# Kernel tuning notes

Hardware: AMD Instinct MI355X
Metric: run time of the kernel (lower is better)

The kernel has to match this reference:

```python
import jax, jax.numpy as jnp
import numpy as np

NJ, NS = 30000, 12000            # num job / skill nodes
E_JS, E_SJ, E_SS = 300000, 300000, 150000
SBERT, HID, OUT = 384, 128, 128
H = 2                             # GAT heads (concat=True)
NEG_SLOPE = 0.2


def setup_inputs() -> dict:
    key = jax.random.key(0)
    ks = iter(jax.random.split(key, 64))
    nrm = lambda shape, s=1.0: jax.random.normal(next(ks), shape, jnp.float32) * s
    ridx = lambda n, hi: jax.random.randint(next(ks), (n,), 0, hi, jnp.int32)
    W = 0.05  # weight scale to keep activations sane across layers
    return dict(
        x_job=nrm((NJ, SBERT)), x_skill=nrm((NS, SBERT)),
        ei_js_src=ridx(E_JS, NJ), ei_js_dst=ridx(E_JS, NS),
        ei_sj_src=ridx(E_SJ, NS), ei_sj_dst=ridx(E_SJ, NJ),
        ei_ss_src=ridx(E_SS, NS), ei_ss_dst=ridx(E_SS, NS),
        query=nrm((SBERT,)),
        W0_job=nrm((SBERT, HID), W), b0_job=jnp.zeros((HID,), jnp.float32),
        g0_job=jnp.ones((HID,), jnp.float32), be0_job=jnp.zeros((HID,), jnp.float32),
        W0_skill=nrm((SBERT, HID), W), b0_skill=jnp.zeros((HID,), jnp.float32),
        g0_skill=jnp.ones((HID,), jnp.float32), be0_skill=jnp.zeros((HID,), jnp.float32),
        gat_Ws=nrm((2, 3, HID, H * HID), W), gat_Wd=nrm((2, 3, HID, H * HID), W),
        gat_as=nrm((2, 3, H, HID), W), gat_ad=nrm((2, 3, H, HID), W),
        gat_b=jnp.zeros((2, 3, H * HID), jnp.float32),
        inter_W=nrm((2, 2, H * HID, HID), W), inter_b=jnp.zeros((2, 2, HID), jnp.float32),
        Wjf=nrm((HID, OUT), W), bjf=jnp.zeros((OUT,), jnp.float32),
        Wq=nrm((SBERT, OUT), W), bq=jnp.zeros((OUT,), jnp.float32),
    )


def _layer_norm(x, g, b):
    mu = x.mean(-1, keepdims=True)
    var = ((x - mu) ** 2).mean(-1, keepdims=True)
    return (x - mu) * jax.lax.rsqrt(var + 1e-5) * g + b


def _gat(x_src, x_dst, src, dst, Ws, Wd, a_s, a_d, bias, num_dst):
    # PyG GATConv: lin_src/lin_dst (no bias), additive attention, scatter-softmax over dst.
    hs = (x_src @ Ws).reshape(-1, H, HID)            # [Ns,H,C]
    hd = (x_dst @ Wd).reshape(-1, H, HID)            # [Nd,H,C]
    e = jax.nn.leaky_relu((hs * a_s).sum(-1)[src] + (hd * a_d).sum(-1)[dst], NEG_SLOPE)  # [E,H]
    m = jax.ops.segment_max(e, dst, num_segments=num_dst)
    p = jnp.exp(e - m[dst])
    den = jax.ops.segment_sum(p, dst, num_segments=num_dst)
    w = p / (den[dst] + 1e-16)                       # [E,H]
    out = jax.ops.segment_sum(hs[src] * w[:, :, None], dst, num_segments=num_dst)
    return out.reshape(num_dst, H * HID) + bias


def _forward(x_job, x_skill, query,
             W0_job, b0_job, g0_job, be0_job, W0_skill, b0_skill, g0_skill, be0_skill,
             gat_Ws, gat_Wd, gat_as, gat_ad, gat_b, inter_W, inter_b, Wjf, bjf, Wq, bq,
             ei_js_src, ei_js_dst, ei_sj_src, ei_sj_dst, ei_ss_src, ei_ss_dst):
    # initial per-type lin + LN + relu (dropout = identity in eval)
    xj = jax.nn.relu(_layer_norm(x_job @ W0_job + b0_job, g0_job, be0_job))
    xs = jax.nn.relu(_layer_norm(x_skill @ W0_skill + b0_skill, g0_skill, be0_skill))
    # skill->skill relation adds self loops (src == dst node type)
    loops = jnp.arange(NS, dtype=jnp.int32)
    ss_src = jnp.concatenate([ei_ss_src, loops])
    ss_dst = jnp.concatenate([ei_ss_dst, loops])
    for i in range(2):  # num_layers
        o_s = (_gat(xj, xs, ei_js_src, ei_js_dst, gat_Ws[i, 0], gat_Wd[i, 0],
                    gat_as[i, 0], gat_ad[i, 0], gat_b[i, 0], NS)
               + _gat(xs, xs, ss_src, ss_dst, gat_Ws[i, 2], gat_Wd[i, 2],
                      gat_as[i, 2], gat_ad[i, 2], gat_b[i, 2], NS))  # HeteroConv aggr='sum'
        o_j = _gat(xs, xj, ei_sj_src, ei_sj_dst, gat_Ws[i, 1], gat_Wd[i, 1],
                   gat_as[i, 1], gat_ad[i, 1], gat_b[i, 1], NJ)
        xj = jax.nn.relu(o_j @ inter_W[i, 0] + inter_b[i, 0])
        xs = jax.nn.relu(o_s @ inter_W[i, 1] + inter_b[i, 1])
    job_emb = xj @ Wjf + bjf                          # [NJ,OUT]
    q = query @ Wq + bq                               # [OUT]
    scores = job_emb @ q                              # [NJ]
    return scores, job_emb, q


def reference(x_job, x_skill, ei_js_src, ei_js_dst, ei_sj_src, ei_sj_dst,
              ei_ss_src, ei_ss_dst, query,
              W0_job, b0_job, g0_job, be0_job, W0_skill, b0_skill, g0_skill, be0_skill,
              gat_Ws, gat_Wd, gat_as, gat_ad, gat_b, inter_W, inter_b,
              Wjf, bjf, Wq, bq):
    return _forward(x_job, x_skill, query,
                    W0_job, b0_job, g0_job, be0_job, W0_skill, b0_skill, g0_skill, be0_skill,
                    gat_Ws, gat_Wd, gat_as, gat_ad, gat_b, inter_W, inter_b, Wjf, bjf, Wq, bq,
                    ei_js_src, ei_js_dst, ei_sj_src, ei_sj_dst, ei_ss_src, ei_ss_dst)
```

## Files before the change

kernel.cpp:

```cpp
#include <hip/hip_runtime.h>
#include <hip/hip_bf16.h>
#include <math.h>

#define NJ 30000
#define NS 12000
#define E_JS 300000
#define E_SJ 300000
#define E_SS 150000
#define ETOT (E_JS + E_SJ + E_SS + NS)
#define NBINS (NS + NJ + NS)
#define NBUK ((NBINS + 63) / 64)
#define SBERT 384
#define HIST_NB 512
#define SCAT_NB 120
#define CAST_MATS 10
#define CAST_BPM 48
#define PREP_CAST (CAST_MATS * CAST_BPM)
#define PREP_WA   (PREP_CAST + 12)
#define PREP_QV   PREP_WA
#define PREP_HIST (PREP_QV + 1)

static inline int cdiv(int a, int b) { return (a + b - 1) / b; }

typedef __attribute__((ext_vector_type(8))) short bf8_t;
typedef __attribute__((ext_vector_type(4))) float f4_t;
typedef unsigned short u16;

__device__ inline float bf2f(unsigned short u) {
    union { unsigned int i; float f; } z; z.i = ((unsigned int)u) << 16; return z.f;
}
__device__ inline unsigned short f2bf(float f) {
    unsigned int x = __float_as_uint(f);
    unsigned int r = (x + 0x7fffu + ((x >> 16) & 1u)) >> 16;
    return (unsigned short)r;
}

__device__ inline void edge_decode(int e, const int* js_src, const int* js_dst,
                                   const int* sj_src, const int* sj_dst,
                                   const int* ss_src, const int* ss_dst,
                                   int& src, int& bin) {
    if (e < E_JS) { src = js_src[e]; bin = js_dst[e]; }
    else if (e < E_JS + E_SJ) { int i = e - E_JS; src = sj_src[i]; bin = NS + sj_dst[i]; }
    else if (e < E_JS + E_SJ + E_SS) { int i = e - E_JS - E_SJ; src = ss_src[i]; bin = NS + NJ + ss_dst[i]; }
    else { int i = e - E_JS - E_SJ - E_SS; src = i; bin = NS + NJ + i; }
}

struct CastT { const float* src; unsigned short* dst; int K; int N; };
struct PrepArgs {
    CastT m[CAST_MATS];
    const float* Ws; const float* as_; const float* Wd; const float* ad_;
    float* wsa; float* wda; int* bcnt;
    const float* query; const float* Wq; const float* bq; float* qv;
    const int* js_src; const int* js_dst;
    const int* sj_src; const int* sj_dst;
    const int* ss_src; const int* ss_dst;
};

__global__ __launch_bounds__(256) void k_prep(PrepArgs A) {
    __shared__ float ldt[32][33];
    __shared__ int lh[NBUK];
    int b = blockIdx.x;
    if (b < PREP_CAST) {
        int mi = b / CAST_BPM, bx = b % CAST_BPM;
        CastT cm = A.m[mi];
        int tilesN = cm.N >> 5;
        int total = (cm.K >> 5) * tilesN;
        if (bx >= total) return;
        int tk = bx / tilesN, tn = bx % tilesN;
        int k0 = tk * 32, n0 = tn * 32;
        int col = threadIdx.x & 31;
        int row0 = threadIdx.x >> 5;
#pragma unroll
        for (int r = 0; r < 4; ++r) {
            int kk = row0 + r * 8;
            ldt[kk][col] = cm.src[(size_t)(k0 + kk) * cm.N + n0 + col];
        }
        __syncthreads();
#pragma unroll
        for (int r = 0; r < 4; ++r) {
            int nn = row0 + r * 8;
            cm.dst[(size_t)(n0 + nn) * cm.K + k0 + col] = f2bf(ldt[col][nn]);
        }
    } else if (b < PREP_WA) {
        int id = (b - PREP_CAST) * 256 + threadIdx.x;
        if (id >= 2 * 1536) return;
        int which = id / 1536;
        int r = id % 1536;
        int lr = r / 256;
        int kh = r % 256;
        int k = kh / 2, h = kh % 2;
        const float* W = which ? A.Wd : A.Ws;
        const float* a = which ? A.ad_ : A.as_;
        const float* wrow = W + ((size_t)(lr * 128 + k)) * 256 + h * 128;
        const float* arow = a + (size_t)(lr * 2 + h) * 128;
        float acc = 0.f;
        for (int c2 = 0; c2 < 128; ++c2) acc += wrow[c2] * arow[c2];
        (which ? A.wda : A.wsa)[lr * 256 + k * 2 + h] = acc;
    } else if (b == PREP_QV) {
        int c = threadIdx.x;
        if (c < 128) {
            float acc = A.bq[c];
            for (int k = 0; k < SBERT; ++k) acc += A.query[k] * A.Wq[(size_t)k * 128 + c];
            A.qv[c] = acc;
        }
    } else {
        int t = threadIdx.x;
        for (int i = t; i < NBUK; i += 256) lh[i] = 0;
        __syncthreads();
        int hb = b - PREP_HIST;
        for (int e = hb * 256 + t; e < ETOT; e += HIST_NB * 256) {
            int src, bin;
            edge_decode(e, A.js_src, A.js_dst, A.sj_src, A.sj_dst, A.ss_src, A.ss_dst, src, bin);
            atomicAdd(&lh[bin >> 6], 1);
        }
        __syncthreads();
        for (int i = t; i < NBUK; i += 256) {
            int v = lh[i];
            if (v) atomicAdd(&A.bcnt[i], v);
        }
    }
}

struct GJob {
    const void* X; const unsigned short* Wt;
    const float* bias; const float* gamma; const float* beta;
    void* Y; int M; int K; int N; int ldY; int srcf32;
    const float* qv; float* sc;
    int aMode = 0;
    const float* wav0 = nullptr; const float* wav1 = nullptr;
    const float* wav2 = nullptr; const float* wav3 = nullptr;
    float* aOut = nullptr; int aStride = 0;
};
struct GPair { GJob a; GJob b; int blocksA; };

template <int EPI>
__device__ void mgemm_body(const GPair& P, int bx, int by) {
    int mb = bx;
    GJob g = (mb < P.blocksA) ? P.a : P.b;
    if (mb >= P.blocksA) mb -= P.blocksA;
    const int n0 = by * 128;
    if (n0 >= g.N) return;
    const int row0 = mb * 64;

    __shared__ __align__(16) unsigned short Al[64][40];
    __shared__ __align__(16) unsigned short Bl[128][40];
    const int t = threadIdx.x;
    const int wave = t >> 6, lane = t & 63;
    const int q = lane >> 4, c = lane & 15;
    const int K = g.K;

    f4_t acc[8];
#pragma unroll
    for (int nt = 0; nt < 8; ++nt) acc[nt] = (f4_t){0.f, 0.f, 0.f, 0.f};

    for (int k0 = 0; k0 < K; k0 += 32) {
#pragma unroll
        for (int it = 0; it < 3; ++it) {
            int idx = t + it * 256;
            int r = idx >> 2, cc = (idx & 3) * 8;
            if (r < 64) {
                int gr = row0 + r;
                if (g.srcf32) {
                    ushort4 lo = make_ushort4(0, 0, 0, 0), hi = lo;
                    if (gr < g.M) {
                        const float* Xf = (const float*)g.X;
                        const float* p = &Xf[(size_t)gr * K + k0 + cc];
                        float4 f0 = *(const float4*)p;
                        float4 f1 = *(const float4*)(p + 4);
                        lo = make_ushort4(f2bf(f0.x), f2bf(f0.y), f2bf(f0.z), f2bf(f0.w));
                        hi = make_ushort4(f2bf(f1.x), f2bf(f1.y), f2bf(f1.z), f2bf(f1.w));
                    }
                    *(ushort4*)&Al[r][cc] = lo;
                    *(ushort4*)&Al[r][cc + 4] = hi;
                } else {
                    const unsigned short* Xb = (const unsigned short*)g.X;
                    uint4 va = (gr < g.M) ? *(const uint4*)&Xb[(size_t)gr * K + k0 + cc]
                                          : make_uint4(0u, 0u, 0u, 0u);
                    *(uint4*)&Al[r][cc] = va;
                }
            } else {
                int br = r - 64;
                *(uint4*)&Bl[br][cc] = *(const uint4*)&g.Wt[(size_t)(n0 + br) * K + k0 + cc];
            }
        }
        __syncthreads();
        bf8_t af = *(const bf8_t*)&Al[wave * 16 + c][q * 8];
#pragma unroll
        for (int nt = 0; nt < 8; ++nt) {
            bf8_t bfr = *(const bf8_t*)&Bl[nt * 16 + c][q * 8];
            acc[nt] = __builtin_amdgcn_mfma_f32_16x16x32_bf16(af, bfr, acc[nt], 0, 0, 0);
        }
        __syncthreads();
    }

    float bcol[8], gcol[8], becol[8], qcol[8];
#pragma unroll
    for (int nt = 0; nt < 8; ++nt) {
        bcol[nt] = (EPI >= 1) ? g.bias[n0 + nt * 16 + c] : 0.f;
        if constexpr (EPI == 3) {
            gcol[nt] = g.gamma[nt * 16 + c];
            becol[nt] = g.beta[nt * 16 + c];
        }
        if constexpr (EPI == 1) qcol[nt] = g.qv[n0 + nt * 16 + c];
    }

#pragma unroll
    for (int r = 0; r < 4; ++r) {
        int grow = row0 + wave * 16 + q * 4 + r;
        float v[8];
#pragma unroll
        for (int nt = 0; nt < 8; ++nt) v[nt] = acc[nt][r] + bcol[nt];
        if constexpr (EPI == 3) {
            float s = 0.f, ss = 0.f;
#pragma unroll
            for (int nt = 0; nt < 8; ++nt) { s += v[nt]; ss += v[nt] * v[nt]; }
#pragma unroll
            for (int m = 8; m >= 1; m >>= 1) {
                s += __shfl_xor(s, m, 64);
                ss += __shfl_xor(ss, m, 64);
            }
            float mu = s * (1.f / 128.f);
            float var = ss * (1.f / 128.f) - mu * mu;
            float rs = rsqrtf(var + 1e-5f);
#pragma unroll
            for (int nt = 0; nt < 8; ++nt)
                v[nt] = fmaxf((v[nt] - mu) * rs * gcol[nt] + becol[nt], 0.f);
        } else if constexpr (EPI == 2) {
#pragma unroll
            for (int nt = 0; nt < 8; ++nt) v[nt] = fmaxf(v[nt], 0.f);
        }
        if constexpr (EPI == 1) {
            float part = 0.f;
#pragma unroll
            for (int nt = 0; nt < 8; ++nt) part += v[nt] * qcol[nt];
#pragma unroll
            for (int m = 8; m >= 1; m >>= 1) part += __shfl_xor(part, m, 64);
            if (c == 0 && grow < g.M) g.sc[grow] = part;
        }
        if (g.aMode > 0) {
            float pa[8];
#pragma unroll
            for (int i = 0; i < 8; ++i) pa[i] = 0.f;
#pragma unroll
            for (int nt = 0; nt < 8; ++nt) {
                int col = nt * 16 + c;
                float2 w0 = *(const float2*)&g.wav0[col * 2];
                pa[0] += v[nt] * w0.x; pa[1] += v[nt] * w0.y;
                if (g.aMode > 1) {
                    float2 w1 = *(const float2*)&g.wav1[col * 2];
                    pa[2] += v[nt] * w1.x; pa[3] += v[nt] * w1.y;
                }
                if (g.aMode > 2) {
                    float2 w2 = *(const float2*)&g.wav2[col * 2];
                    float2 w3 = *(const float2*)&g.wav3[col * 2];
                    pa[4] += v[nt] * w2.x; pa[5] += v[nt] * w2.y;
                    pa[6] += v[nt] * w3.x; pa[7] += v[nt] * w3.y;
                }
            }
#pragma unroll
            for (int m = 8; m >= 1; m >>= 1) {
                pa[0] += __shfl_xor(pa[0], m, 64); pa[1] += __shfl_xor(pa[1], m, 64);
                pa[2] += __shfl_xor(pa[2], m, 64); pa[3] += __shfl_xor(pa[3], m, 64);
                pa[4] += __shfl_xor(pa[4], m, 64); pa[5] += __shfl_xor(pa[5], m, 64);
                pa[6] += __shfl_xor(pa[6], m, 64); pa[7] += __shfl_xor(pa[7], m, 64);
            }
            if (c == 0 && grow < g.M) {
                float* ao = &g.aOut[(size_t)grow * g.aStride];
                ao[0] = pa[0]; ao[1] = pa[1];
                if (g.aMode > 1) { ao[2] = pa[2]; ao[3] = pa[3]; }
                if (g.aMode > 2) { ao[4] = pa[4]; ao[5] = pa[5]; ao[6] = pa[6]; ao[7] = pa[7]; }
            }
        }
        if (grow < g.M) {
            if constexpr (EPI == 1) {
                float* Y = (float*)g.Y;
#pragma unroll
                for (int nt = 0; nt < 8; ++nt)
                    Y[(size_t)grow * g.ldY + n0 + nt * 16 + c] = v[nt];
            } else {
                unsigned short* Y = (unsigned short*)g.Y;
#pragma unroll
                for (int nt = 0; nt < 8; ++nt)
                    Y[(size_t)grow * g.ldY + n0 + nt * 16 + c] = f2bf(v[nt]);
            }
        }
    }
}

template <int EPI>
__global__ __launch_bounds__(256) void k_mgemm(GPair P) {
    mgemm_body<EPI>(P, blockIdx.x, blockIdx.y);
}

__global__ __launch_bounds__(256) void k_lin0_scan(
    GPair P, int gemmBlocks,
    const int* __restrict__ bcnt, int* __restrict__ bukoff, int* __restrict__ bukcur) {
    if (blockIdx.x < (unsigned)gemmBlocks) {
        mgemm_body<3>(P, blockIdx.x, 0);
        return;
    }
    __shared__ int sd[256];
    int t = threadIdx.x;
    int i0 = t * 4;
    int v0 = (i0 < NBUK) ? bcnt[i0] : 0;
    int v1 = (i0 + 1 < NBUK) ? bcnt[i0 + 1] : 0;
    int v2 = (i0 + 2 < NBUK) ? bcnt[i0 + 2] : 0;
    int v3 = (i0 + 3 < NBUK) ? bcnt[i0 + 3] : 0;
    int csum = v0 + v1 + v2 + v3;
    sd[t] = csum;
    __syncthreads();
    for (int off = 1; off < 256; off <<= 1) {
        int tmp = (t >= off) ? sd[t - off] : 0;
        __syncthreads();
        sd[t] += tmp;
        __syncthreads();
    }
    int excl = sd[t] - csum;
    int p0 = excl, p1 = excl + v0, p2 = excl + v0 + v1, p3 = excl + v0 + v1 + v2;
    if (i0 < NBUK) { bukoff[i0] = p0; bukcur[i0] = p0; }
    if (i0 + 1 < NBUK) { bukoff[i0 + 1] = p1; bukcur[i0 + 1] = p1; }
    if (i0 + 2 < NBUK) { bukoff[i0 + 2] = p2; bukcur[i0 + 2] = p2; }
    if (i0 + 3 < NBUK) { bukoff[i0 + 3] = p3; bukcur[i0 + 3] = p3; }
    if (t == 0) bukoff[NBUK] = ETOT;
}

__global__ __launch_bounds__(256) void k_scatter_proj(
    GPair P, int gemmBlocks,
    const int* __restrict__ js_src, const int* __restrict__ js_dst,
    const int* __restrict__ sj_src, const int* __restrict__ sj_dst,
    const int* __restrict__ ss_src, const int* __restrict__ ss_dst,
    int* __restrict__ bukcur, uint2* __restrict__ pairs) {
    if (blockIdx.x < (unsigned)gemmBlocks) {
        mgemm_body<0>(P, blockIdx.x, blockIdx.y);
        return;
    }
    if (blockIdx.y != 0) return;
    __shared__ int lh[NBUK];
    __shared__ int lbase[NBUK];
    int t = threadIdx.x;
    int sb = blockIdx.x - gemmBlocks;
    const int CH = (ETOT + SCAT_NB - 1) / SCAT_NB;
    const int beg = sb * CH;
    const int endi = (beg + CH < ETOT) ? beg + CH : ETOT;
    for (int i = t; i < NBUK; i += 256) lh[i] = 0;
    __syncthreads();
    for (int e = beg + t; e < endi; e += 256) {
        int src, bin;
        edge_decode(e, js_src, js_dst, sj_src, sj_dst, ss_src, ss_dst, src, bin);
        atomicAdd(&lh[bin >> 6], 1);
    }
    __syncthreads();
    for (int i = t; i < NBUK; i += 256) {
        int v = lh[i];
        lbase[i] = v ? atomicAdd(&bukcur[i], v) : 0;
    }
    __syncthreads();
    for (int i = t; i < NBUK; i += 256) lh[i] = 0;
    __syncthreads();
    for (int e = beg + t; e < endi; e += 256) {
        int src, bin;
        edge_decode(e, js_src, js_dst, sj_src, sj_dst, ss_src, ss_dst, src, bin);
        int bu = bin >> 6;
        int pos = lbase[bu] + atomicAdd(&lh[bu], 1);
        pairs[pos] = make_uint2((unsigned)src, (unsigned)bin);
    }
}

__global__ __launch_bounds__(256) void k_finalize(
    const uint2* __restrict__ pairs, const int* __restrict__ bukoff,
    int* __restrict__ offs, int* __restrict__ esrc) {
    int b = blockIdx.x, t = threadIdx.x;
    int base = bukoff[b], endi = bukoff[b + 1];
    __shared__ int cnt[64], excl[64], curs[64];
    if (t < 64) cnt[t] = 0;
    __syncthreads();
    for (int i = base + t; i < endi; i += 256)
        atomicAdd(&cnt[pairs[i].y & 63], 1);
    __syncthreads();
    if (t < 64) {
        int v = cnt[t];
        int inc = v;
#pragma unroll
        for (int off = 1; off < 64; off <<= 1) {
            int tmp = __shfl_up(inc, off, 64);
            if (t >= off) inc += tmp;
        }
        excl[t] = inc - v;
        curs[t] = inc - v;
    }
    __syncthreads();
    for (int i = base + t; i < endi; i += 256) {
        uint2 p = pairs[i];
        int lb = p.y & 63;
        int pos = atomicAdd(&curs[lb], 1);
        esrc[base + pos] = (int)p.x;
    }
    if (t < 64) {
        int bin = b * 64 + t;
        if (bin < NBINS) offs[bin] = base + excl[t];
    }
    if (b == 0 && t == 0) offs[NBINS] = ETOT;
}

__device__ inline void fmacc8(float p, uint4 u, float acc[8]) {
    acc[0] += p * __uint_as_float(u.x << 16);
    acc[1] += p * __uint_as_float(u.x & 0xffff0000u);
    acc[2] += p * __uint_as_float(u.y << 16);
    acc[3] += p * __uint_as_float(u.y & 0xffff0000u);
    acc[4] += p * __uint_as_float(u.z << 16);
    acc[5] += p * __uint_as_float(u.z & 0xffff0000u);
    acc[6] += p * __uint_as_float(u.w << 16);
    acc[7] += p * __uint_as_float(u.w & 0xffff0000u);
}

__device__ inline void rel_run(
    const int* __restrict__ esrc, int beg, int cnt,
    const float* __restrict__ aSrc, int aShift, int aOff, float ad,
    const unsigned short* __restrict__ hs, int ldShift, int colBase, int half,
    float acc[8], float& den) {
    int n2 = cnt & ~1;
    int j = beg;
    for (; j + 4 <= beg + n2; j += 4) {
        int sA = esrc[j + half];
        int sB = esrc[j + 2 + half];
        uint4 uA = *(const uint4*)&hs[((size_t)sA << ldShift) + colBase];
        uint4 uB = *(const uint4*)&hs[((size_t)sB << ldShift) + colBase];
        float aA = aSrc[((size_t)sA << aShift) + aOff];
        float aB = aSrc[((size_t)sB << aShift) + aOff];
        float eA = aA + ad; eA = eA > 0.f ? eA : 0.2f * eA;
        float eB = aB + ad; eB = eB > 0.f ? eB : 0.2f * eB;
        float pA = __expf(eA), pB = __expf(eB);
        fmacc8(pA, uA, acc);
        fmacc8(pB, uB, acc);
        den += pA + pB;
    }
    for (; j < beg + n2; j += 2) {
        int s = esrc[j + half];
        uint4 u = *(const uint4*)&hs[((size_t)s << ldShift) + colBase];
        float a = aSrc[((size_t)s << aShift) + aOff];
        float e = a + ad; e = e > 0.f ? e : 0.2f * e;
        float p = __expf(e);
        fmacc8(p, u, acc);
        den += p;
    }
    if (cnt & 1) {
        if (!half) {
            int s = esrc[beg + cnt - 1];
            uint4 u = *(const uint4*)&hs[((size_t)s << ldShift) + colBase];
            float a = aSrc[((size_t)s << aShift) + aOff];
            float e = a + ad; e = e > 0.f ? e : 0.2f * e;
            float p = __expf(e);
            fmacc8(p, u, acc);
            den += p;
        }
    }
}

__device__ inline void reduce_scale(float acc[8], float& den, float out[8], int add) {
    float d = den + __shfl_xor(den, 32, 64);
    float sc = 1.f / (d + 1e-16f);
#pragma unroll
    for (int i = 0; i < 8; ++i) {
        float t = acc[i] + __shfl_xor(acc[i], 32, 64);
        if (add) out[i] += t * sc; else out[i] = t * sc;
    }
}

__device__ inline void store8(unsigned short* dst, const float v[8]) {
    uint4 o;
    o.x = (unsigned)f2bf(v[0]) | ((unsigned)f2bf(v[1]) << 16);
    o.y = (unsigned)f2bf(v[2]) | ((unsigned)f2bf(v[3]) << 16);
    o.z = (unsigned)f2bf(v[4]) | ((unsigned)f2bf(v[5]) << 16);
    o.w = (unsigned)f2bf(v[6]) | ((unsigned)f2bf(v[7]) << 16);
    *(uint4*)dst = o;
}

__global__ __launch_bounds__(256) void k_gather_all(
    const int* __restrict__ offs, const int* __restrict__ esrc,
    const float* __restrict__ aJ, const float* __restrict__ aS,
    const unsigned short* __restrict__ hs1,
    const unsigned short* __restrict__ hsss, int ssShift,
    const unsigned short* __restrict__ hsj, int sjShift,
    const float* __restrict__ gb,
    unsigned short* __restrict__ oj, unsigned short* __restrict__ os,
    int jobOnly) {
    int wave = threadIdx.x >> 6, lane = threadIdx.x & 63;
    int idx = blockIdx.x * 4 + wave;
    int half = lane >> 5;
    int colBase = (lane & 31) * 8;
    int myH = (colBase >= 128) ? 1 : 0;

    float acc[8], den, out[8];
#pragma unroll
    for (int i = 0; i < 8; ++i) acc[i] = 0.f;
    den = 0.f;

    if (jobOnly) {
        if (idx >= NJ) return;
        int d = idx;
        int bb = NS + d;
        int beg = offs[bb], cnt = offs[bb + 1] - beg;
        float ad = aJ[(size_t)d * 4 + 2 + myH];
        rel_run(esrc, beg, cnt, aS, 3, 4 + myH, ad, hsj, sjShift, colBase, half, acc, den);
        reduce_scale(acc, den, out, 0);
        if (half == 0) {
            float4 b0 = *(const float4*)&gb[256 + colBase];
            float4 b1 = *(const float4*)&gb[256 + colBase + 4];
            out[0] += b0.x; out[1] += b0.y; out[2] += b0.z; out[3] += b0.w;
            out[4] += b1.x; out[5] += b1.y; out[6] += b1.z; out[7] += b1.w;
            store8(&oj[(size_t)d * 256 + colBase], out);
        }
        return;
    }
    if (idx < NS) {
        int d = idx;
        int beg = offs[d], cnt = offs[d + 1] - beg;
        float adA = aS[(size_t)d * 8 + 2 + myH];
        rel_run(esrc, beg, cnt, aJ, 2, myH, adA, hs1, 8, colBase, half, acc, den);
        reduce_scale(acc, den, out, 0);
#pragma unroll
        for (int i = 0; i < 8; ++i) acc[i] = 0.f;
        den = 0.f;
        int bb = NS + NJ + d;
        int beg2 = offs[bb], cnt2 = offs[bb + 1] - beg2;
        float adB = aS[(size_t)d * 8 + 6 + myH];
        rel_run(esrc, beg2, cnt2, aS, 3, myH, adB, hsss, ssShift, colBase, half, acc, den);
        reduce_scale(acc, den, out, 1);
        if (half == 0) {
            float4 bA0 = *(const float4*)&gb[colBase];
            float4 bA1 = *(const float4*)&gb[colBase + 4];
            float4 bB0 = *(const float4*)&gb[512 + colBase];
            float4 bB1 = *(const float4*)&gb[512 + colBase + 4];
            out[0] += bA0.x + bB0.x; out[1] += bA0.y + bB0.y;
            out[2] += bA0.z + bB0.z; out[3] += bA0.w + bB0.w;
            out[4] += bA1.x + bB1.x; out[5] += bA1.y + bB1.y;
            out[6] += bA1.z + bB1.z; out[7] += bA1.w + bB1.w;
            store8(&os[(size_t)d * 256 + colBase], out);
        }
    } else if (idx < NS + NJ) {
        int d = idx - NS;
        int bb = NS + d;
        int beg = offs[bb], cnt = offs[bb + 1] - beg;
        float ad = aJ[(size_t)d * 4 + 2 + myH];
        rel_run(esrc, beg, cnt, aS, 3, 4 + myH, ad, hsj, sjShift, colBase, half, acc, den);
        reduce_scale(acc, den, out, 0);
        if (half == 0) {
            float4 b0 = *(const float4*)&gb[256 + colBase];
            float4 b1 = *(const float4*)&gb[256 + colBase + 4];
            out[0] += b0.x; out[1] += b0.y; out[2] += b0.z; out[3] += b0.w;
            out[4] += b1.x; out[5] += b1.y; out[6] += b1.z; out[7] += b1.w;
            store8(&oj[(size_t)d * 256 + colBase], out);
        }
    }
}

struct FJob {
    const unsigned short* X; const unsigned short* Wt1; const float* bias1;
    int M; int K1;
    const float* wa; float* aOut; int aStride;
    const unsigned short* Wt2; const float* bias2; int N2;
    void* Y2; int ldY2; int y2f32;
    const float* qv; float* sc;
};
struct FPair { FJob a; FJob b; int blocksA; };

__global__ __launch_bounds__(256) void k_fused2(FPair P) {
    int mb = blockIdx.x;
    FJob g = (mb < P.blocksA) ? P.a : P.b;
    if (mb >= P.blocksA) mb -= P.blocksA;
    const int row0 = mb * 64;

    __shared__ __align__(16) unsigned short Al[64][40];
    __shared__ __align__(16) unsigned short Bl[128][40];
    __shared__ __align__(16) unsigned short Y1l[4][64][40];
    const int t = threadIdx.x;
    const int wave = t >> 6, lane = t & 63;
    const int q = lane >> 4, c = lane & 15;

    f4_t acc[8];
#pragma unroll
    for (int nt = 0; nt < 8; ++nt) acc[nt] = (f4_t){0.f, 0.f, 0.f, 0.f};

    for (int k0 = 0; k0 < g.K1; k0 += 32) {
#pragma unroll
        for (int it = 0; it < 3; ++it) {
            int idx = t + it * 256;
            int r = idx >> 2, cc = (idx & 3) * 8;
            if (r < 64) {
                int gr = row0 + r;
                uint4 va = (gr < g.M) ? *(const uint4*)&g.X[(size_t)gr * g.K1 + k0 + cc]
                                      : make_uint4(0u, 0u, 0u, 0u);
                *(uint4*)&Al[r][cc] = va;
            } else {
                int br = r - 64;
                *(uint4*)&Bl[br][cc] = *(const uint4*)&g.Wt1[(size_t)br * g.K1 + k0 + cc];
            }
        }
        __syncthreads();
        bf8_t af = *(const bf8_t*)&Al[wave * 16 + c][q * 8];
#pragma unroll
        for (int nt = 0; nt < 8; ++nt) {
            bf8_t bfr = *(const bf8_t*)&Bl[nt * 16 + c][q * 8];
            acc[nt] = __builtin_amdgcn_mfma_f32_16x16x32_bf16(af, bfr, acc[nt], 0, 0, 0);
        }
        __syncthreads();
    }

    float bcol[8];
#pragma unroll
    for (int nt = 0; nt < 8; ++nt) bcol[nt] = g.bias1[nt * 16 + c];
#pragma unroll
    for (int r = 0; r < 4; ++r) {
        int row = wave * 16 + q * 4 + r;
        int grow = row0 + row;
        float v[8];
#pragma unroll
        for (int nt = 0; nt < 8; ++nt) v[nt] = fmaxf(acc[nt][r] + bcol[nt], 0.f);
        if (g.wa) {
            float pa0 = 0.f, pa1 = 0.f;
#pragma unroll
            for (int nt = 0; nt < 8; ++nt) {
                float2 w0 = *(const float2*)&g.wa[(nt * 16 + c) * 2];
                pa0 += v[nt] * w0.x; pa1 += v[nt] * w0.y;
            }
#pragma unroll
            for (int m = 8; m >= 1; m >>= 1) {
                pa0 += __shfl_xor(pa0, m, 64);
                pa1 += __shfl_xor(pa1, m, 64);
            }
            if (c == 0 && grow < g.M) {
                g.aOut[(size_t)grow * g.aStride + 0] = pa0;
                g.aOut[(size_t)grow * g.aStride + 1] = pa1;
            }
        }
#pragma unroll
        for (int nt = 0; nt < 8; ++nt)
            Y1l[nt >> 1][row][(nt & 1) * 16 + c] = f2bf(v[nt]);
    }
    if (g.N2 == 0) return;
    __syncthreads();

    for (int n2 = 0; n2 < g.N2; n2 += 128) {
        f4_t acc2[8];
#pragma unroll
        for (int nt = 0; nt < 8; ++nt) acc2[nt] = (f4_t){0.f, 0.f, 0.f, 0.f};
        for (int k0 = 0; k0 < 128; k0 += 32) {
#pragma unroll
            for (int it = 0; it < 2; ++it) {
                int idx = t + it * 256;
                int br = idx >> 2, cc = (idx & 3) * 8;
                *(uint4*)&Bl[br][cc] = *(const uint4*)&g.Wt2[(size_t)(n2 + br) * 128 + k0 + cc];
            }
            __syncthreads();
            bf8_t af = *(const bf8_t*)&Y1l[k0 >> 5][wave * 16 + c][q * 8];
#pragma unroll
            for (int nt = 0; nt < 8; ++nt) {
                bf8_t bfr = *(const bf8_t*)&Bl[nt * 16 + c][q * 8];
                acc2[nt] = __builtin_amdgcn_mfma_f32_16x16x32_bf16(af, bfr, acc2[nt], 0, 0, 0);
            }
            __syncthreads();
        }
        float b2[8], qcol[8];
#pragma unroll
        for (int nt = 0; nt < 8; ++nt) {
            b2[nt] = g.bias2 ? g.bias2[n2 + nt * 16 + c] : 0.f;
            if (g.y2f32) qcol[nt] = g.qv[n2 + nt * 16 + c];
        }
#pragma unroll
        for (int r = 0; r < 4; ++r) {
            int grow = row0 + wave * 16 + q * 4 + r;
            float v[8];
#pragma unroll
            for (int nt = 0; nt < 8; ++nt) v[nt] = acc2[nt][r] + b2[nt];
            if (g.y2f32) {
                float part = 0.f;
#pragma unroll
                for (int nt = 0; nt < 8; ++nt) part += v[nt] * qcol[nt];
#pragma unroll
                for (int m = 8; m >= 1; m >>= 1) part += __shfl_xor(part, m, 64);
                if (c == 0 && grow < g.M) g.sc[grow] = part;
                if (grow < g.M) {
                    float* Y = (float*)g.Y2;
#pragma unroll
                    for (int nt = 0; nt < 8; ++nt)
                        Y[(size_t)grow * g.ldY2 + n2 + nt * 16 + c] = v[nt];
                }
            } else if (grow < g.M) {
                unsigned short* Y = (unsigned short*)g.Y2;
#pragma unroll
                for (int nt = 0; nt < 8; ++nt)
                    Y[(size_t)grow * g.ldY2 + n2 + nt * 16 + c] = f2bf(v[nt]);
            }
        }
    }
}

extern "C" void kernel_launch(void* const* d_in, const int* in_sizes, int n_in,
                              void* d_out, int out_size, void* d_ws, size_t ws_size,
                              hipStream_t stream) {
    const float* x_job   = (const float*)d_in[0];
    const float* x_skill = (const float*)d_in[1];
    const int* js_src = (const int*)d_in[2];
    const int* js_dst = (const int*)d_in[3];
    const int* sj_src = (const int*)d_in[4];
    const int* sj_dst = (const int*)d_in[5];
    const int* ss_src = (const int*)d_in[6];
    const int* ss_dst = (const int*)d_in[7];
    const float* query    = (const float*)d_in[8];
    const float* W0_job   = (const float*)d_in[9];
    const float* b0_job   = (const float*)d_in[10];
    const float* g0_job   = (const float*)d_in[11];
    const float* be0_job  = (const float*)d_in[12];
    const float* W0_skill = (const float*)d_in[13];
    const float* b0_skill = (const float*)d_in[14];
    const float* g0_skill = (const float*)d_in[15];
    const float* be0_skill= (const float*)d_in[16];
    const float* gat_Ws = (const float*)d_in[17];
    const float* gat_Wd = (const float*)d_in[18];
    const float* gat_as = (const float*)d_in[19];
    const float* gat_ad = (const float*)d_in[20];
    const float* gat_b  = (const float*)d_in[21];
    const float* inter_W = (const float*)d_in[22];
    const float* inter_b = (const float*)d_in[23];
    const float* Wjf = (const float*)d_in[24];
    const float* bjf = (const float*)d_in[25];
    const float* Wq  = (const float*)d_in[26];
    const float* bq  = (const float*)d_in[27];

    char* w = (char*)d_ws;
    auto alloc = [&](size_t bytes) -> void* {
        void* p = (void*)w;
        w += (bytes + 255) & ~(size_t)255;
        return p;
    };
    u16* xj  = (u16*)alloc((size_t)NJ * 128 * 2);
    u16* xs  = (u16*)alloc((size_t)NS * 128 * 2);
    u16* hs1 = (u16*)alloc((size_t)NJ * 256 * 2);
    u16* hs2 = (u16*)alloc((size_t)NS * 512 * 2);
    u16* hs3 = (u16*)alloc((size_t)NS * 256 * 2);
    u16* oj  = (u16*)alloc((size_t)NJ * 256 * 2);
    u16* os  = (u16*)alloc((size_t)NS * 256 * 2);
    u16* WtW0j = (u16*)alloc((size_t)SBERT * 128 * 2);
    u16* WtW0s = (u16*)alloc((size_t)SBERT * 128 * 2);
    u16* WtWs  = (u16*)alloc((size_t)6 * 128 * 256 * 2);
    u16* WtI   = (u16*)alloc((size_t)4 * 256 * 128 * 2);
    u16* WtJf  = (u16*)alloc((size_t)128 * 128 * 2);
    float* aJ = (float*)alloc((size_t)NJ * 4 * 4);
    float* aS = (float*)alloc((size_t)NS * 8 * 4);
    float* wsa = (float*)alloc(6 * 256 * 4);
    float* wda = (float*)alloc(6 * 256 * 4);
    int* bcnt   = (int*)alloc((size_t)NBUK * 4);
    int* bukoff = (int*)alloc((size_t)(NBUK + 1) * 4);
    int* bukcur = (int*)alloc((size_t)NBUK * 4);
    uint2* pairs = (uint2*)alloc((size_t)ETOT * 8);
    int* offs = (int*)alloc((size_t)(NBINS + 1) * 4);
    int* esrc = (int*)alloc((size_t)ETOT * 4);

    float* out = (float*)d_out;
    float* scores  = out;
    float* job_emb = out + NJ;
    float* qv      = out + NJ + (size_t)NJ * 128;

    const int mbJ = cdiv(NJ, 64);
    const int mbS = cdiv(NS, 64);
    const int gemmB = mbJ + mbS;

    hipMemsetAsync(bcnt, 0, (size_t)NBUK * 4, stream);

    {
        PrepArgs A;
        A.m[0] = {W0_job, WtW0j, SBERT, 128};
        A.m[1] = {W0_skill, WtW0s, SBERT, 128};
        A.m[2] = {gat_Ws + (size_t)0 * 128 * 256, WtWs + (size_t)0 * 256 * 128, 128, 256};
        A.m[3] = {gat_Ws + (size_t)1 * 128 * 256, WtWs + (size_t)1 * 256 * 128, 128, 256};
        A.m[4] = {gat_Ws + (size_t)2 * 128 * 256, WtWs + (size_t)2 * 256 * 128, 128, 256};
        A.m[5] = {gat_Ws + (size_t)4 * 128 * 256, WtWs + (size_t)4 * 256 * 128, 128, 256};
        A.m[6] = {inter_W + (size_t)0 * 256 * 128, WtI + (size_t)0 * 128 * 256, 256, 128};
        A.m[7] = {inter_W + (size_t)1 * 256 * 128, WtI + (size_t)1 * 128 * 256, 256, 128};
        A.m[8] = {inter_W + (size_t)2 * 256 * 128, WtI + (size_t)2 * 128 * 256, 256, 128};
        A.m[9] = {Wjf, WtJf, 128, 128};
        A.Ws = gat_Ws; A.as_ = gat_as; A.Wd = gat_Wd; A.ad_ = gat_ad;
        A.wsa = wsa; A.wda = wda; A.bcnt = bcnt;
        A.query = query; A.Wq = Wq; A.bq = bq; A.qv = qv;
        A.js_src = js_src; A.js_dst = js_dst;
        A.sj_src = sj_src; A.sj_dst = sj_dst;
        A.ss_src = ss_src; A.ss_dst = ss_dst;
        k_prep<<<PREP_HIST + HIST_NB, 256, 0, stream>>>(A);
    }

    {
        GPair P;
        P.a = {x_job, WtW0j, b0_job, g0_job, be0_job, xj, NJ, SBERT, 128, 128, 1,
               nullptr, nullptr, 2, wsa + 0, wda + 256, nullptr, nullptr, aJ, 4};
        P.b = {x_skill, WtW0s, b0_skill, g0_skill, be0_skill, xs, NS, SBERT, 128, 128, 1,
               nullptr, nullptr, 4, wsa + 2 * 256, wda + 0, wsa + 1 * 256, wda + 2 * 256, aS, 8};
        P.blocksA = mbJ;
        k_lin0_scan<<<dim3(gemmB + 1, 1), 256, 0, stream>>>(P, gemmB, bcnt, bukoff, bukcur);
    }

    {
        GPair P;
        P.a = {xj, WtWs + (size_t)0 * 256 * 128, nullptr, nullptr, nullptr,
               hs1, NJ, 128, 256, 256, 0, nullptr, nullptr};
        P.b = {xs, WtWs + (size_t)1 * 256 * 128, nullptr, nullptr, nullptr,
               hs2, NS, 128, 512, 512, 0, nullptr, nullptr};
        P.blocksA = mbJ;
        k_scatter_proj<<<dim3(gemmB + SCAT_NB, 4), 256, 0, stream>>>(
            P, gemmB, js_src, js_dst, sj_src, sj_dst, ss_src, ss_dst, bukcur, pairs);
    }

    k_finalize<<<NBUK, 256, 0, stream>>>(pairs, bukoff, offs, esrc);

    k_gather_all<<<cdiv(NS + NJ, 4), 256, 0, stream>>>(
        offs, esrc, aJ, aS, hs1, hs2 + 256, 9, hs2, 9, gat_b, oj, os, 0);

    {
        FPair P;
        P.a = {oj, WtI + (size_t)0 * 128 * 256, inter_b + 0, NJ, 256,
               wda + (size_t)4 * 256, aJ + 2, 4,
               nullptr, nullptr, 0, nullptr, 0, 0, nullptr, nullptr};
        P.b = {os, WtI + (size_t)1 * 128 * 256, inter_b + 128, NS, 256,
               wsa + (size_t)4 * 256, aS + 4, 8,
               WtWs + (size_t)4 * 256 * 128, nullptr, 256, hs3, 256, 0, nullptr, nullptr};
        P.blocksA = mbJ;
        k_fused2<<<dim3(gemmB, 1), 256, 0, stream>>>(P);
    }

    k_gather_all<<<cdiv(NJ, 4), 256, 0, stream>>>(
        offs, esrc, aJ, aS, nullptr, nullptr, 8, hs3, 8,
        gat_b + (size_t)3 * 256, oj, nullptr, 1);

    {
        FPair P;
        P.a = {oj, WtI + (size_t)2 * 128 * 256, inter_b + 2 * 128, NJ, 256,
               nullptr, nullptr, 0,
               WtJf, bjf, 128, job_emb, 128, 1, qv, scores};
        P.b = P.a;
        P.blocksA = mbJ;
        k_fused2<<<dim3(mbJ, 1), 256, 0, stream>>>(P);
    }
}
```

Before: 349.7 us.

## Split GAT gather across 8 column groups with 8 edges per wave

```diff
diff --git a/kernel.cpp b/kernel.cpp
--- a/kernel.cpp
+++ b/kernel.cpp
@@ -402,77 +402,49 @@
     if (b == 0 && t == 0) offs[NBINS] = ETOT;
 }
 
-__device__ inline void fmacc8(float p, uint4 u, float acc[8]) {
-    acc[0] += p * __uint_as_float(u.x << 16);
-    acc[1] += p * __uint_as_float(u.x & 0xffff0000u);
-    acc[2] += p * __uint_as_float(u.y << 16);
-    acc[3] += p * __uint_as_float(u.y & 0xffff0000u);
-    acc[4] += p * __uint_as_float(u.z << 16);
-    acc[5] += p * __uint_as_float(u.z & 0xffff0000u);
-    acc[6] += p * __uint_as_float(u.w << 16);
-    acc[7] += p * __uint_as_float(u.w & 0xffff0000u);
-}
-
 __device__ inline void rel_run(
-    const int* __restrict__ esrc, int beg, int cnt,
+    const int* __restrict__ esrc, int beg, int end,
     const float* __restrict__ aSrc, int aShift, int aOff, float ad,
-    const unsigned short* __restrict__ hs, int ldShift, int colBase, int half,
-    float acc[8], float& den) {
-    int n2 = cnt & ~1;
-    int j = beg;
-    for (; j + 4 <= beg + n2; j += 4) {
-        int sA = esrc[j + half];
-        int sB = esrc[j + 2 + half];
-        uint4 uA = *(const uint4*)&hs[((size_t)sA << ldShift) + colBase];
-        uint4 uB = *(const uint4*)&hs[((size_t)sB << ldShift) + colBase];
-        float aA = aSrc[((size_t)sA << aShift) + aOff];
-        float aB = aSrc[((size_t)sB << aShift) + aOff];
-        float eA = aA + ad; eA = eA > 0.f ? eA : 0.2f * eA;
-        float eB = aB + ad; eB = eB > 0.f ? eB : 0.2f * eB;
-        float pA = __expf(eA), pB = __expf(eB);
-        fmacc8(pA, uA, acc);
-        fmacc8(pB, uB, acc);
-        den += pA + pB;
-    }
-    for (; j < beg + n2; j += 2) {
-        int s = esrc[j + half];
-        uint4 u = *(const uint4*)&hs[((size_t)s << ldShift) + colBase];
-        float a = aSrc[((size_t)s << aShift) + aOff];
-        float e = a + ad; e = e > 0.f ? e : 0.2f * e;
-        float p = __expf(e);
-        fmacc8(p, u, acc);
+    const unsigned short* __restrict__ hs, int ldShift, int colOff, int g,
+    float acc[4], float& den) {
+    for (int j = beg; j < end; j += 8) {
+        int e = j + g;
+        bool ok = e < end;
+        int ee = ok ? e : beg;
+        int s = esrc[ee];
+        uint2 u = *(const uint2*)&hs[((unsigned)s << ldShift) + colOff];
+        float a = aSrc[((unsigned)s << aShift) + aOff];
+        float x = a + ad; x = x > 0.f ? x : 0.2f * x;
+        float p = ok ? __expf(x) : 0.f;
+        acc[0] += p * __uint_as_float(u.x << 16);
+        acc[1] += p * __uint_as_float(u.x & 0xffff0000u);
+        acc[2] += p * __uint_as_float(u.y << 16);
+        acc[3] += p * __uint_as_float(u.y & 0xffff0000u);
         den += p;
     }
-    if (cnt & 1) {
-        if (!half) {
-            int s = esrc[beg + cnt - 1];
-            uint4 u = *(const uint4*)&hs[((size_t)s << ldShift) + colBase];
-            float a = aSrc[((size_t)s << aShift) + aOff];
-            float e = a + ad; e = e > 0.f ? e : 0.2f * e;
-            float p = __expf(e);
-            fmacc8(p, u, acc);
-            den += p;
-        }
-    }
-}
-
-__device__ inline void reduce_scale(float acc[8], float& den, float out[8], int add) {
-    float d = den + __shfl_xor(den, 32, 64);
+}
+
+__device__ inline void reduce_scale4(float acc[4], float& den, float out[4], int add) {
+    float d = den;
+    d += __shfl_xor(d, 8, 64);
+    d += __shfl_xor(d, 16, 64);
+    d += __shfl_xor(d, 32, 64);
     float sc = 1.f / (d + 1e-16f);
 #pragma unroll
-    for (int i = 0; i < 8; ++i) {
-        float t = acc[i] + __shfl_xor(acc[i], 32, 64);
+    for (int i = 0; i < 4; ++i) {
+        float t = acc[i];
+        t += __shfl_xor(t, 8, 64);
+        t += __shfl_xor(t, 16, 64);
+        t += __shfl_xor(t, 32, 64);
         if (add) out[i] += t * sc; else out[i] = t * sc;
     }
 }
 
-__device__ inline void store8(unsigned short* dst, const float v[8]) {
-    uint4 o;
+__device__ inline void store4(unsigned short* dst, const float v[4]) {
+    uint2 o;
     o.x = (unsigned)f2bf(v[0]) | ((unsigned)f2bf(v[1]) << 16);
     o.y = (unsigned)f2bf(v[2]) | ((unsigned)f2bf(v[3]) << 16);
-    o.z = (unsigned)f2bf(v[4]) | ((unsigned)f2bf(v[5]) << 16);
-    o.w = (unsigned)f2bf(v[6]) | ((unsigned)f2bf(v[7]) << 16);
-    *(uint4*)dst = o;
+    *(uint2*)dst = o;
 }
 
 __global__ __launch_bounds__(256) void k_gather_all(
@@ -485,71 +457,61 @@
     unsigned short* __restrict__ oj, unsigned short* __restrict__ os,
     int jobOnly) {
     int wave = threadIdx.x >> 6, lane = threadIdx.x & 63;
-    int idx = blockIdx.x * 4 + wave;
-    int half = lane >> 5;
-    int colBase = (lane & 31) * 8;
-    int myH = (colBase >= 128) ? 1 : 0;
-
-    float acc[8], den, out[8];
-#pragma unroll
-    for (int i = 0; i < 8; ++i) acc[i] = 0.f;
-    den = 0.f;
+    int cg = blockIdx.x & 7;
+    int idx = (blockIdx.x >> 3) * 4 + wave;
+    int g = lane >> 3, cl = lane & 7;
+    int colOff = cg * 32 + cl * 4;
+    int myH = cg >> 2;
+
+    float acc[4] = {0.f, 0.f, 0.f, 0.f}, out[4];
+    float den = 0.f;
 
     if (jobOnly) {
         if (idx >= NJ) return;
         int d = idx;
         int bb = NS + d;
-        int beg = offs[bb], cnt = offs[bb + 1] - beg;
-        float ad = aJ[(size_t)d * 4 + 2 + myH];
-        rel_run(esrc, beg, cnt, aS, 3, 4 + myH, ad, hsj, sjShift, colBase, half, acc, den);
-        reduce_scale(acc, den, out, 0);
-        if (half == 0) {
-            float4 b0 = *(const float4*)&gb[256 + colBase];
-            float4 b1 = *(const float4*)&gb[256 + colBase + 4];
+        int beg = offs[bb], end = offs[bb + 1];
+        float ad = aJ[(unsigned)d * 4 + 2 + myH];
+        rel_run(esrc, beg, end, aS, 3, 4 + myH, ad, hsj, sjShift, colOff, g, acc, den);
+        reduce_scale4(acc, den, out, 0);
+        if (g == 0) {
+            float4 b0 = *(const float4*)&gb[256 + colOff];
             out[0] += b0.x; out[1] += b0.y; out[2] += b0.z; out[3] += b0.w;
-            out[4] += b1.x; out[5] += b1.y; out[6] += b1.z; out[7] += b1.w;
-            store8(&oj[(size_t)d * 256 + colBase], out);
+            store4(&oj[(size_t)d * 256 + colOff], out);
         }
         return;
     }
     if (idx < NS) {
         int d = idx;
-        int beg = offs[d], cnt = offs[d + 1] - beg;
-        float adA = aS[(size_t)d * 8 + 2 + myH];
-        rel_run(esrc, beg, cnt, aJ, 2, myH, adA, hs1, 8, colBase, half, acc, den);
-        reduce_scale(acc, den, out, 0);
-#pragma unroll
-        for (int i = 0; i < 8; ++i) acc[i] = 0.f;
+        int beg = offs[d], end = offs[d + 1];
+        float adA = aS[(unsigned)d * 8 + 2 + myH];
+        rel_run(esrc, beg, end, aJ, 2, myH, adA, hs1, 8, colOff, g, acc, den);
+        reduce_scale4(acc, den, out, 0);
+        acc[0] = acc[1] = acc[2] = acc[3] = 0.f;
         den = 0.f;
         int bb = NS + NJ + d;
-        int beg2 = offs[bb], cnt2 = offs[bb + 1] - beg2;
-        float adB = aS[(size_t)d * 8 + 6 + myH];
-        rel_run(esrc, beg2, cnt2, aS, 3, myH, adB, hsss, ssShift, colBase, half, acc, den);
-        reduce_scale(acc, den, out, 1);
-        if (half == 0) {
-            float4 bA0 = *(const float4*)&gb[colBase];
-            float4 bA1 = *(const float4*)&gb[colBase + 4];
-            float4 bB0 = *(const float4*)&gb[512 + colBase];
-            float4 bB1 = *(const float4*)&gb[512 + colBase + 4];
-            out[0] += bA0.x + bB0.x; out[1] += bA0.y + bB0.y;
-            out[2] += bA0.z + bB0.z; out[3] += bA0.w + bB0.w;
-            out[4] += bA1.x + bB1.x; out[5] += bA1.y + bB1.y;
-            out[6] += bA1.z + bB1.z; out[7] += bA1.w + bB1.w;
-            store8(&os[(size_t)d * 256 + colBase], out);
+        int beg2 = offs[bb], end2 = offs[bb + 1];
+        float adB = aS[(unsigned)d * 8 + 6 + myH];
+        rel_run(esrc, beg2, end2, aS, 3, myH, adB, hsss, ssShift, colOff, g, acc, den);
+        reduce_scale4(acc, den, out, 1);
+        if (g == 0) {
+            float4 bA = *(const float4*)&gb[colOff];
+            float4 bB = *(const float4*)&gb[512 + colOff];
+            out[0] += bA.x + bB.x; out[1] += bA.y + bB.y;
+            out[2] += bA.z + bB.z; out[3] += bA.w + bB.w;
+            store4(&os[(size_t)d * 256 + colOff], out);
         }
     } else if (idx < NS + NJ) {
         int d = idx - NS;
         int bb = NS + d;
-        int beg = offs[bb], cnt = offs[bb + 1] - beg;
-        float ad = aJ[(size_t)d * 4 + 2 + myH];
-        rel_run(esrc, beg, cnt, aS, 3, 4 + myH, ad, hsj, sjShift, colBase, half, acc, den);
-        reduce_scale(acc, den, out, 0);
-        if (half == 0) {
-            float4 b0 = *(const float4*)&gb[256 + colBase];
-            float4 b1 = *(const float4*)&gb[256 + colBase + 4];
+        int beg = offs[bb], end = offs[bb + 1];
+        float ad = aJ[(unsigned)d * 4 + 2 + myH];
+        rel_run(esrc, beg, end, aS, 3, 4 + myH, ad, hsj, sjShift, colOff, g, acc, den);
+        reduce_scale4(acc, den, out, 0);
+        if (g == 0) {
+            float4 b0 = *(const float4*)&gb[256 + colOff];
             out[0] += b0.x; out[1] += b0.y; out[2] += b0.z; out[3] += b0.w;
-            out[4] += b1.x; out[5] += b1.y; out[6] += b1.z; out[7] += b1.w;
-            store8(&oj[(size_t)d * 256 + colBase], out);
+            store4(&oj[(size_t)d * 256 + colOff], out);
         }
     }
 }
@@ -811,7 +773,7 @@
 
     k_finalize<<<NBUK, 256, 0, stream>>>(pairs, bukoff, offs, esrc);
 
-    k_gather_all<<<cdiv(NS + NJ, 4), 256, 0, stream>>>(
+    k_gather_all<<<8 * cdiv(NS + NJ, 4), 256, 0, stream>>>(
         offs, esrc, aJ, aS, hs1, hs2 + 256, 9, hs2, 9, gat_b, oj, os, 0);
 
     {
@@ -826,7 +788,7 @@
         k_fused2<<<dim3(gemmB, 1), 256, 0, stream>>>(P);
     }
 
-    k_gather_all<<<cdiv(NJ, 4), 256, 0, stream>>>(
+    k_gather_all<<<8 * cdiv(NJ, 4), 256, 0, stream>>>(
         offs, esrc, aJ, aS, nullptr, nullptr, 8, hs3, 8,
         gat_b + (size_t)3 * 256, oj, nullptr, 1);
 
```

Result: slower. 488.2 us (+39.6%).
